# Optimization experiments

Measured on AMD Instinct MI355X. Metric: run time of the kernel, lower is better.

Reference implementation:

```python
import jax, jax.numpy as jnp
import numpy as np

B, T, D, E, K = 2, 2048, 1024, 8, 2
H = 2 * D  # expert hidden

def setup_inputs() -> dict:
    key = jax.random.key(0)
    ks = jax.random.split(key, 5)
    s = 0.02
    return {
        "x": jax.random.normal(ks[0], (B, T, D), jnp.float32),
        "Wr": jax.random.normal(ks[1], (D, E), jnp.float32) * s,
        "br": jnp.zeros((E,), jnp.float32),
        "W1": jax.random.normal(ks[2], (E, D, H), jnp.float32) * s,
        "b1": jnp.zeros((E, H), jnp.float32),
        "W2": jax.random.normal(ks[3], (E, H, D), jnp.float32) * s,
        "b2": jnp.zeros((E, D), jnp.float32),
    }

def reference(x, Wr, br, W1, b1, W2, b2):
    # Router: logits -> top-k -> sparse softmax gates (non-top-k get 0 weight)
    logits = jnp.einsum('btd,de->bte', x, Wr) + br            # [B,T,E]
    topv, topi = jax.lax.top_k(logits, K)                      # [B,T,K]
    sel_mask = (jax.nn.one_hot(topi, E, dtype=logits.dtype).sum(-2) > 0)  # [B,T,E]
    neg_inf = jnp.finfo(logits.dtype).min
    gates = jax.nn.softmax(jnp.where(sel_mask, logits, neg_inf), axis=-1)  # [B,T,E], zero off top-k
    # Experts: final = sum_e gate[...,e] * Expert_e(x). Gate is exactly 0 for
    # non-selected experts, so dense-per-expert compute gives identical math to
    # the gather/scatter loop in the torch module. Dropout is identity (eval).
    h = jax.nn.relu(jnp.einsum('btd,edh->bteh', x, W1) + b1)   # [B,T,E,H]
    out = jnp.einsum('bte,bteh,ehd->btd', gates, h, W2)
    out = out + jnp.einsum('bte,ed->btd', gates, b2)
    return out
```

## Files before the change

kernel.cpp:

```cpp
#include <hip/hip_runtime.h>
#include <hip/hip_bf16.h>
#include <math.h>

namespace {

constexpr int NTOK   = 4096;
constexpr int DDIM   = 1024;
constexpr int E      = 8;
constexpr int HDIM   = 2048;
constexpr int MAXROWS = 8192;
constexpr int MAXBLK  = 56;

typedef __bf16 bf16;
typedef __attribute__((ext_vector_type(8))) __bf16 bf16x8;
typedef __attribute__((ext_vector_type(4))) float floatx4;
typedef __attribute__((ext_vector_type(4))) int   i32x4;

__device__ inline void gload_lds16(const bf16* g, bf16* l) {
  __builtin_amdgcn_global_load_lds(
      (const __attribute__((address_space(1))) void*)g,
      (__attribute__((address_space(3))) void*)l, 16, 0, 0);
}

__device__ inline bf16x8 ds_read16(const bf16* p) {
  i32x4 r;
  asm volatile("ds_read_b128 %0, %1"
               : "=v"(r)
               : "v"((const __attribute__((address_space(3))) bf16*)p));
  return __builtin_bit_cast(bf16x8, r);
}

__device__ inline unsigned short bfbits(float f) {
  return __builtin_bit_cast(unsigned short, (bf16)f);
}

__device__ inline void transpose_tile256(const float* __restrict__ src,
                                         bf16* __restrict__ dst,
                                         int R, int C, int c0, int r0,
                                         unsigned short (*tileT)[264]) {
  int tid = threadIdx.x;
  int rp = (tid >> 4) * 2;
  int tc = (tid & 15) * 4;
#pragma unroll
  for (int i = 0; i < 8; ++i) {
    int r = rp + i * 32;
    float4 v0 = *(const float4*)(src + (size_t)(r0 + r)     * C + c0 + tc);
    float4 v1 = *(const float4*)(src + (size_t)(r0 + r + 1) * C + c0 + tc);
    *(unsigned int*)&tileT[tc + 0][r] = (unsigned int)bfbits(v0.x) | ((unsigned int)bfbits(v1.x) << 16);
    *(unsigned int*)&tileT[tc + 1][r] = (unsigned int)bfbits(v0.y) | ((unsigned int)bfbits(v1.y) << 16);
    *(unsigned int*)&tileT[tc + 2][r] = (unsigned int)bfbits(v0.z) | ((unsigned int)bfbits(v1.z) << 16);
    *(unsigned int*)&tileT[tc + 3][r] = (unsigned int)bfbits(v0.w) | ((unsigned int)bfbits(v1.w) << 16);
  }
  __syncthreads();
  int tc2 = (tid & 31) * 8;
  int tr2 = tid >> 5;
#pragma unroll
  for (int i = 0; i < 8; ++i) {
    int c = tr2 + i * 8;
    *(bf16x8*)(dst + (size_t)(c0 + c) * R + r0 + tc2) =
        *(const bf16x8*)&tileT[c][tc2];
  }
}

__global__ __launch_bounds__(256) void prep_kernel(
    const float* __restrict__ x,  const float* __restrict__ Wr,
    const float* __restrict__ br, const float* __restrict__ W1,
    const float* __restrict__ W2,
    int* __restrict__ topk_e, float* __restrict__ topk_g,
    bf16* __restrict__ xb, bf16* __restrict__ W1T, bf16* __restrict__ W2T) {
  __shared__ unsigned short tileT[64][264];
  int b = blockIdx.x;
  if (b < 1024) {
    int bx = b & 31, by = (b >> 5) & 3, bz = b >> 7;
    const float* src = W1 + (size_t)bz * DDIM * HDIM;
    bf16* dst = W1T + (size_t)bz * DDIM * HDIM;
    transpose_tile256(src, dst, DDIM, HDIM, bx * 64, by * 256, tileT);
    return;
  }
  if (b < 2048) {
    int lb = b - 1024;
    int bx = lb & 15, by = (lb >> 4) & 7, bz = lb >> 7;
    const float* src = W2 + (size_t)bz * DDIM * HDIM;
    bf16* dst = W2T + (size_t)bz * DDIM * HDIM;
    transpose_tile256(src, dst, HDIM, DDIM, bx * 64, by * 256, tileT);
    return;
  }
  int rb = b - 2048;
  int wave = threadIdx.x >> 6;
  int lane = threadIdx.x & 63;
  int t0 = (rb * 4 + wave) * 2;

  float acc[16];
#pragma unroll
  for (int j = 0; j < 16; ++j) acc[j] = 0.f;

#pragma unroll
  for (int i = 0; i < DDIM / 64; ++i) {
    int d = i * 64 + lane;
    float4 w0 = *(const float4*)(Wr + (size_t)d * E);
    float4 w1 = *(const float4*)(Wr + (size_t)d * E + 4);
#pragma unroll
    for (int t = 0; t < 2; ++t) {
      float xv = x[(size_t)(t0 + t) * DDIM + d];
      xb[(size_t)(t0 + t) * DDIM + d] = (bf16)xv;
      acc[t * 8 + 0] += xv * w0.x; acc[t * 8 + 1] += xv * w0.y;
      acc[t * 8 + 2] += xv * w0.z; acc[t * 8 + 3] += xv * w0.w;
      acc[t * 8 + 4] += xv * w1.x; acc[t * 8 + 5] += xv * w1.y;
      acc[t * 8 + 6] += xv * w1.z; acc[t * 8 + 7] += xv * w1.w;
    }
  }
#pragma unroll
  for (int off = 32; off > 0; off >>= 1) {
#pragma unroll
    for (int j = 0; j < 16; ++j) acc[j] += __shfl_xor(acc[j], off, 64);
  }
  if (lane == 0) {
#pragma unroll
    for (int t = 0; t < 2; ++t) {
      int tt = t0 + t;
      float lg[E];
#pragma unroll
      for (int e = 0; e < E; ++e) lg[e] = acc[t * 8 + e] + br[e];
      int e0 = 0;
#pragma unroll
      for (int e = 1; e < E; ++e) if (lg[e] > lg[e0]) e0 = e;
      int e1 = (e0 == 0) ? 1 : 0;
#pragma unroll
      for (int e = 0; e < E; ++e) if (e != e0 && lg[e] > lg[e1]) e1 = e;
      float ex = expf(lg[e1] - lg[e0]);
      float s = 1.f + ex;
      topk_e[2 * tt]     = e0;
      topk_e[2 * tt + 1] = e1;
      topk_g[2 * tt]     = 1.f / s;
      topk_g[2 * tt + 1] = ex / s;
    }
  }
}

__global__ __launch_bounds__(1024) void scan_scatter_kernel(
    const int* __restrict__ topk_e,
    int* __restrict__ counts,
    int* __restrict__ offsets,
    int* __restrict__ blockmap,
    int* __restrict__ rowtok, int* __restrict__ tokrow) {
  __shared__ int hist[E], curs[E];
  int tid = threadIdx.x;
  int lane = tid & 63;
  unsigned long long lt = ((unsigned long long)1 << lane) - 1;
  if (tid < E) hist[tid] = 0;
  __syncthreads();
  for (int i = tid; i < 2 * NTOK; i += 1024) {
    int e = topk_e[i];
#pragma unroll
    for (int ee = 0; ee < E; ++ee) {
      unsigned long long m = __ballot(e == ee);
      if (m && lane == __ffsll((long long)m) - 1) atomicAdd(&hist[ee], __popcll(m));
    }
  }
  __syncthreads();
  if (tid == 0) {
    int live[MAXBLK];
    int s = 0, nb = 0;
    for (int e = 0; e < E; ++e) {
      int c = hist[e];
      curs[e] = s;
      counts[e * 16] = c;
      offsets[e] = s;
      int nt = (c + 191) / 192;
      for (int m = 0; m < nt; ++m) live[nb++] = (e << 16) | m;
      s += c;
    }
    offsets[E] = s;
    for (int xc = 0; xc < 8; ++xc) {
      int lo = (nb * xc) >> 3, hi = (nb * (xc + 1)) >> 3;
      for (int j = 0; j < 7; ++j)
        blockmap[7 * xc + j] = (lo + j < hi) ? live[lo + j] : -1;
    }
  }
  __syncthreads();
  for (int i = tid; i < 2 * NTOK; i += 1024) {
    int e = topk_e[i];
#pragma unroll
    for (int ee = 0; ee < E; ++ee) {
      unsigned long long m = __ballot(e == ee);
      if (m) {
        int leader = __ffsll((long long)m) - 1;
        int base = 0;
        if (lane == leader) base = atomicAdd(&curs[ee], __popcll(m));
        base = __shfl(base, leader, 64);
        if (e == ee) {
          int row = base + __popcll(m & lt);
          rowtok[row] = i >> 1;
          tokrow[i] = row;
        }
      }
    }
  }
}

template <bool GATHER, bool RELU>
__global__ __launch_bounds__(256, 2) void ffn_gemm(
    const bf16* __restrict__ A, const bf16* __restrict__ W,
    const float* __restrict__ bias, bf16* __restrict__ Y,
    const int* __restrict__ rowtok, const int* __restrict__ offsets,
    const int* __restrict__ counts,
    const int* __restrict__ blockmap,
    int Kdim, int Ndim) {
  static_assert(MAXBLK == 56, "XCD chunking assumes gridDim.x == 56 == 8*7");
  int xcd = blockIdx.x & 7;
  int mq  = blockIdx.x >> 3;
  int bm = blockmap[xcd * 7 + mq];
  if (bm < 0) return;
  int e = bm >> 16;
  int mBase = (bm & 0xffff) * 192;
  int cnt = counts[e * 16];
  int rowBase = offsets[e] + mBase;
  int nBase = blockIdx.y * 128;
  int validRows = cnt - mBase; if (validRows > 192) validRows = 192;

  __shared__ bf16 Asm[2][192 * 64];
  __shared__ bf16 Bsm[2][128 * 64];

  int tid = threadIdx.x;
  int wave = tid >> 6, lane = tid & 63;
  int lrow = lane >> 3;
  int lseg = lane & 7;
  int sseg = lseg ^ lrow;

  const bf16* aptr[6];
  const bf16* bptr[4];
#pragma unroll
  for (int i = 0; i < 6; ++i) {
    int c = wave + i * 4;
    int r = rowBase + c * 8 + lrow;
    if (r > MAXROWS - 1) r = MAXROWS - 1;
    size_t rowoff = GATHER ? (size_t)rowtok[r] * Kdim : (size_t)r * Kdim;
    aptr[i] = A + rowoff + sseg * 8;
  }
#pragma unroll
  for (int i = 0; i < 4; ++i) {
    int c = wave + i * 4;
    bptr[i] = W + ((size_t)e * Ndim + nBase + c * 8 + lrow) * (size_t)Kdim + sseg * 8;
  }

  floatx4 acc[6][4];
#pragma unroll
  for (int m = 0; m < 6; ++m)
#pragma unroll
    for (int n = 0; n < 4; ++n) acc[m][n] = floatx4{0.f, 0.f, 0.f, 0.f};

  int wm = wave & 1, wn = wave >> 1;
  int mrow = lane & 15;
  int kseg0 = lane >> 4;
  int swz = mrow & 7;

  auto issue = [&](int p, int kc) {
#pragma unroll
    for (int i = 0; i < 6; ++i) {
      int c = wave + i * 4;
      gload_lds16(aptr[i] + kc, &Asm[p][c * 512]);
    }
#pragma unroll
    for (int i = 0; i < 4; ++i) {
      int c = wave + i * 4;
      gload_lds16(bptr[i] + kc, &Bsm[p][c * 512]);
    }
  };

  issue(0, 0);
  int p = 0;
  for (int kc = 0; kc < Kdim; kc += 64) {
    if (kc + 64 < Kdim) {
      issue(p ^ 1, kc + 64);
      asm volatile("s_waitcnt vmcnt(10)" ::: "memory");
    } else {
      asm volatile("s_waitcnt vmcnt(0)" ::: "memory");
    }
    asm volatile("s_barrier" ::: "memory");

#pragma unroll
    for (int ks = 0; ks < 2; ++ks) {
      int kk = (((ks << 2) | kseg0) ^ swz) << 3;
      bf16x8 af[6], bfr[4];
#pragma unroll
      for (int m = 0; m < 6; ++m)
        af[m] = ds_read16(&Asm[p][(wm * 96 + m * 16 + mrow) * 64 + kk]);
#pragma unroll
      for (int n = 0; n < 4; ++n)
        bfr[n] = ds_read16(&Bsm[p][(wn * 64 + n * 16 + mrow) * 64 + kk]);
      asm volatile("s_waitcnt lgkmcnt(0)" ::: "memory");
      __builtin_amdgcn_sched_barrier(0);
      __builtin_amdgcn_s_setprio(1);
#pragma unroll
      for (int m = 0; m < 6; ++m)
#pragma unroll
        for (int n = 0; n < 4; ++n)
          acc[m][n] = __builtin_amdgcn_mfma_f32_16x16x32_bf16(af[m], bfr[n], acc[m][n], 0, 0, 0);
      __builtin_amdgcn_s_setprio(0);
    }

    asm volatile("s_barrier" ::: "memory");
    p ^= 1;
  }

  int crow = (lane >> 4) * 4;
  int ccol = lane & 15;
#pragma unroll
  for (int n = 0; n < 4; ++n) {
    int colg = nBase + wn * 64 + n * 16 + ccol;
    float bv = bias[(size_t)e * Ndim + colg];
#pragma unroll
    for (int m = 0; m < 6; ++m) {
#pragma unroll
      for (int r = 0; r < 4; ++r) {
        int rl = wm * 96 + m * 16 + crow + r;
        if (rl < validRows) {
          float v = acc[m][n][r] + bv;
          if (RELU) v = fmaxf(v, 0.f);
          Y[(size_t)(rowBase + rl) * Ndim + colg] = (bf16)v;
        }
      }
    }
  }
}

__global__ void combine_kernel(const bf16* __restrict__ Y2,
                               const int* __restrict__ tokrow,
                               const float* __restrict__ topk_g,
                               float* __restrict__ out) {
  int idx = blockIdx.x * 256 + threadIdx.x;
  int t = idx >> 7;
  int d8 = (idx & 127) * 8;
  int r0 = tokrow[2 * t], r1 = tokrow[2 * t + 1];
  float g0 = topk_g[2 * t], g1 = topk_g[2 * t + 1];
  bf16x8 a = *(const bf16x8*)(Y2 + (size_t)r0 * DDIM + d8);
  bf16x8 b = *(const bf16x8*)(Y2 + (size_t)r1 * DDIM + d8);
  float o[8];
#pragma unroll
  for (int j = 0; j < 8; ++j) o[j] = g0 * (float)a[j] + g1 * (float)b[j];
  float* op = out + (size_t)t * DDIM + d8;
  *(float4*)op = *(float4*)&o[0];
  *(float4*)(op + 4) = *(float4*)&o[4];
}

}

extern "C" void kernel_launch(void* const* d_in, const int* in_sizes, int n_in,
                              void* d_out, int out_size, void* d_ws, size_t ws_size,
                              hipStream_t stream) {
  const float* x  = (const float*)d_in[0];
  const float* Wr = (const float*)d_in[1];
  const float* br = (const float*)d_in[2];
  const float* W1 = (const float*)d_in[3];
  const float* b1 = (const float*)d_in[4];
  const float* W2 = (const float*)d_in[5];
  const float* b2 = (const float*)d_in[6];
  float* out = (float*)d_out;

  char* w = (char*)d_ws;
  int*   counts   = (int*)(w);
  int*   offsets  = (int*)(w + 1024);
  int*   blockmap = (int*)(w + 2048);
  int*   topk_e   = (int*)(w + 4096);
  float* topk_g   = (float*)(w + 4096 + 32768);
  int*   rowtok   = (int*)(w + 4096 + 65536);
  int*   tokrow   = (int*)(w + 4096 + 98304);
  char*  big      = w + 4096 + 131072;
  bf16* xb  = (bf16*)(big);
  bf16* W1T = (bf16*)(big + 8388608);
  bf16* W2T = (bf16*)(big + 8388608 + 33554432);
  bf16* Y1  = (bf16*)(big + 8388608 + 67108864);
  bf16* Y2  = (bf16*)(big + 8388608);

  prep_kernel<<<2560, 256, 0, stream>>>(x, Wr, br, W1, W2, topk_e, topk_g, xb, W1T, W2T);
  scan_scatter_kernel<<<1, 1024, 0, stream>>>(topk_e, counts, offsets, blockmap,
                                              rowtok, tokrow);
  ffn_gemm<true, true><<<dim3(MAXBLK, HDIM / 128), 256, 0, stream>>>(
      xb, W1T, b1, Y1, rowtok, offsets, counts, blockmap, DDIM, HDIM);
  ffn_gemm<false, false><<<dim3(MAXBLK, DDIM / 128), 256, 0, stream>>>(
      Y1, W2T, b2, Y2, rowtok, offsets, counts, blockmap, HDIM, DDIM);
  combine_kernel<<<NTOK * DDIM / 8 / 256, 256, 0, stream>>>(Y2, tokrow, topk_g, out);
}
```

Measured before the change: 349.3 us.

## Shrink weight-transpose tiles, XOR-swizzle LDS, parallelize scan blockmap build

```diff
diff --git a/kernel.cpp b/kernel.cpp
--- a/kernel.cpp
+++ b/kernel.cpp
@@ -34,31 +34,42 @@
   return __builtin_bit_cast(unsigned short, (bf16)f);
 }
 
-__device__ inline void transpose_tile256(const float* __restrict__ src,
+__device__ inline void transpose_tile128(const float* __restrict__ src,
                                          bf16* __restrict__ dst,
                                          int R, int C, int c0, int r0,
-                                         unsigned short (*tileT)[264]) {
+                                         unsigned short (*tileT)[136]) {
   int tid = threadIdx.x;
   int rp = (tid >> 4) * 2;
   int tc = (tid & 15) * 4;
-#pragma unroll
-  for (int i = 0; i < 8; ++i) {
+  float4 v0[4], v1[4];
+#pragma unroll
+  for (int i = 0; i < 4; ++i) {
     int r = rp + i * 32;
-    float4 v0 = *(const float4*)(src + (size_t)(r0 + r)     * C + c0 + tc);
-    float4 v1 = *(const float4*)(src + (size_t)(r0 + r + 1) * C + c0 + tc);
-    *(unsigned int*)&tileT[tc + 0][r] = (unsigned int)bfbits(v0.x) | ((unsigned int)bfbits(v1.x) << 16);
-    *(unsigned int*)&tileT[tc + 1][r] = (unsigned int)bfbits(v0.y) | ((unsigned int)bfbits(v1.y) << 16);
-    *(unsigned int*)&tileT[tc + 2][r] = (unsigned int)bfbits(v0.z) | ((unsigned int)bfbits(v1.z) << 16);
-    *(unsigned int*)&tileT[tc + 3][r] = (unsigned int)bfbits(v0.w) | ((unsigned int)bfbits(v1.w) << 16);
+    v0[i] = *(const float4*)(src + (size_t)(r0 + r)     * C + c0 + tc);
+    v1[i] = *(const float4*)(src + (size_t)(r0 + r + 1) * C + c0 + tc);
+  }
+#pragma unroll
+  for (int i = 0; i < 4; ++i) {
+    int r = rp + i * 32;
+#pragma unroll
+    for (int q = 0; q < 4; ++q) {
+      int c = tc + q;
+      int xorv = ((c >> 2) & 7) << 3;
+      float a = ((const float*)&v0[i])[q];
+      float b = ((const float*)&v1[i])[q];
+      *(unsigned int*)&tileT[c][r ^ xorv] =
+          (unsigned int)bfbits(a) | ((unsigned int)bfbits(b) << 16);
+    }
   }
   __syncthreads();
-  int tc2 = (tid & 31) * 8;
-  int tr2 = tid >> 5;
-#pragma unroll
-  for (int i = 0; i < 8; ++i) {
-    int c = tr2 + i * 8;
+  int tc2 = (tid & 15) * 8;
+  int tr2 = tid >> 4;
+#pragma unroll
+  for (int i = 0; i < 4; ++i) {
+    int c = tr2 + i * 16;
+    int xorv = ((c >> 2) & 7) << 3;
     *(bf16x8*)(dst + (size_t)(c0 + c) * R + r0 + tc2) =
-        *(const bf16x8*)&tileT[c][tc2];
+        *(const bf16x8*)&tileT[c][tc2 ^ xorv];
   }
 }
 
@@ -68,24 +79,24 @@
     const float* __restrict__ W2,
     int* __restrict__ topk_e, float* __restrict__ topk_g,
     bf16* __restrict__ xb, bf16* __restrict__ W1T, bf16* __restrict__ W2T) {
-  __shared__ unsigned short tileT[64][264];
+  __shared__ unsigned short tileT[64][136];
   int b = blockIdx.x;
-  if (b < 1024) {
-    int bx = b & 31, by = (b >> 5) & 3, bz = b >> 7;
+  if (b < 2048) {
+    int bx = b & 31, by = (b >> 5) & 7, bz = b >> 8;
     const float* src = W1 + (size_t)bz * DDIM * HDIM;
     bf16* dst = W1T + (size_t)bz * DDIM * HDIM;
-    transpose_tile256(src, dst, DDIM, HDIM, bx * 64, by * 256, tileT);
+    transpose_tile128(src, dst, DDIM, HDIM, bx * 64, by * 128, tileT);
     return;
   }
-  if (b < 2048) {
-    int lb = b - 1024;
-    int bx = lb & 15, by = (lb >> 4) & 7, bz = lb >> 7;
+  if (b < 4096) {
+    int lb = b - 2048;
+    int bx = lb & 15, by = (lb >> 4) & 15, bz = lb >> 8;
     const float* src = W2 + (size_t)bz * DDIM * HDIM;
     bf16* dst = W2T + (size_t)bz * DDIM * HDIM;
-    transpose_tile256(src, dst, HDIM, DDIM, bx * 64, by * 256, tileT);
+    transpose_tile128(src, dst, HDIM, DDIM, bx * 64, by * 128, tileT);
     return;
   }
-  int rb = b - 2048;
+  int rb = b - 4096;
   int wave = threadIdx.x >> 6;
   int lane = threadIdx.x & 63;
   int t0 = (rb * 4 + wave) * 2;
@@ -158,24 +169,29 @@
     }
   }
   __syncthreads();
-  if (tid == 0) {
-    int live[MAXBLK];
-    int s = 0, nb = 0;
-    for (int e = 0; e < E; ++e) {
-      int c = hist[e];
-      curs[e] = s;
-      counts[e * 16] = c;
-      offsets[e] = s;
-      int nt = (c + 191) / 192;
-      for (int m = 0; m < nt; ++m) live[nb++] = (e << 16) | m;
-      s += c;
-    }
-    offsets[E] = s;
-    for (int xc = 0; xc < 8; ++xc) {
-      int lo = (nb * xc) >> 3, hi = (nb * (xc + 1)) >> 3;
-      for (int j = 0; j < 7; ++j)
-        blockmap[7 * xc + j] = (lo + j < hi) ? live[lo + j] : -1;
-    }
+  int h[E], pre[E + 1], nt[E], tb[E + 1];
+  pre[0] = 0; tb[0] = 0;
+#pragma unroll
+  for (int e = 0; e < E; ++e) {
+    h[e] = hist[e];
+    pre[e + 1] = pre[e] + h[e];
+    nt[e] = (h[e] + 191) / 192;
+    tb[e + 1] = tb[e] + nt[e];
+  }
+  int nb = tb[E];
+  if (tid < E) { counts[tid * 16] = h[tid]; curs[tid] = pre[tid]; }
+  if (tid < E + 1) offsets[tid] = pre[tid];
+  if (tid < MAXBLK) {
+    int xc = tid / 7, j = tid % 7;
+    int lo = (nb * xc) >> 3, hi = (nb * (xc + 1)) >> 3;
+    int idx = lo + j, v = -1;
+    if (idx < hi) {
+      int e = 0;
+#pragma unroll
+      for (int k = 1; k < E; ++k) if (idx >= tb[k]) e = k;
+      v = (e << 16) | (idx - tb[e]);
+    }
+    blockmap[tid] = v;
   }
   __syncthreads();
   for (int i = tid; i < 2 * NTOK; i += 1024) {
@@ -372,7 +388,7 @@
   bf16* Y1  = (bf16*)(big + 8388608 + 67108864);
   bf16* Y2  = (bf16*)(big + 8388608);
 
-  prep_kernel<<<2560, 256, 0, stream>>>(x, Wr, br, W1, W2, topk_e, topk_g, xb, W1T, W2T);
+  prep_kernel<<<4608, 256, 0, stream>>>(x, Wr, br, W1, W2, topk_e, topk_g, xb, W1T, W2T);
   scan_scatter_kernel<<<1, 1024, 0, stream>>>(topk_e, counts, offsets, blockmap,
                                               rowtok, tokrow);
   ffn_gemm<true, true><<<dim3(MAXBLK, HDIM / 128), 256, 0, stream>>>(
```

Result: faster. 329.6 us (-5.6%).
